# Kernel optimization log

Measured on AMD Instinct MI355X. Metric: run time of the kernel, lower is better.

Reference implementation:

```python
import jax, jax.numpy as jnp
import numpy as np

N_NODES = 100000
N_EDGES = 1280000
D_IN = 64
D_HID = 128
D_OUT = 64


def sage_conv(x, src, dst, W_l, b_l, W_r, n_nodes):
    # PyG SAGEConv (aggr='mean', root_weight=True):
    #   out_i = W_l @ mean_{j in N(i)} x_j + b_l + W_r @ x_i
    msg = x[src]  # [E, d] gather of source-node features
    agg = jax.ops.segment_sum(msg, dst, num_segments=n_nodes)  # [N, d]
    cnt = jax.ops.segment_sum(jnp.ones((src.shape[0], 1), x.dtype), dst,
                              num_segments=n_nodes)  # [N, 1]
    mean = agg / jnp.maximum(cnt, 1.0)  # zero-neighbor nodes -> 0 (matches scatter-mean)
    return mean @ W_l.T + b_l + x @ W_r.T


def setup_inputs() -> dict:
    key = jax.random.key(0)
    ks = jax.random.split(key, 8)
    x = jax.random.normal(ks[0], (N_NODES, D_IN), dtype=jnp.float32)
    edge_index = jax.random.randint(ks[1], (2, N_EDGES), 0, N_NODES, dtype=jnp.int64)
    s = 0.05
    W_l1 = jax.random.normal(ks[2], (D_HID, D_IN), dtype=jnp.float32) * s
    b_l1 = jnp.zeros((D_HID,), dtype=jnp.float32)
    W_r1 = jax.random.normal(ks[3], (D_HID, D_IN), dtype=jnp.float32) * s
    W_l2 = jax.random.normal(ks[4], (D_OUT, D_HID), dtype=jnp.float32) * s
    b_l2 = jnp.zeros((D_OUT,), dtype=jnp.float32)
    W_r2 = jax.random.normal(ks[5], (D_OUT, D_HID), dtype=jnp.float32) * s
    return {"x": x, "edge_index": edge_index,
            "W_l1": W_l1, "b_l1": b_l1, "W_r1": W_r1,
            "W_l2": W_l2, "b_l2": b_l2, "W_r2": W_r2}


def reference(x, edge_index, W_l1, b_l1, W_r1, W_l2, b_l2, W_r2):
    src, dst = edge_index[0], edge_index[1]
    n = x.shape[0]
    h = sage_conv(x, src, dst, W_l1, b_l1, W_r1, n)
    h = jax.nn.relu(h)
    out = sage_conv(h, src, dst, W_l2, b_l2, W_r2, n)
    return out
```

## Files before the change

kernel.cpp:

```cpp
#include <hip/hip_runtime.h>
#include <cstdint>
#include <cstddef>

typedef __attribute__((ext_vector_type(8))) short short8;
typedef __attribute__((ext_vector_type(4))) float floatx4;

static constexpr int DIN  = 64;
static constexpr int DHID = 128;
static constexpr int BSH  = 7;
static constexpr int BNODES = 1 << BSH;
static constexpr int TILE = 8192;
static constexpr int CAP  = 4096;
static constexpr unsigned SENT = 0xFFFFFFFFu;

__device__ inline short f2bf(float f) {
  unsigned u = __float_as_uint(f);
  u += 0x7FFF + ((u >> 16) & 1);
  return (short)(u >> 16);
}
__device__ inline float bf2f(short s) {
  return __uint_as_float(((unsigned)(unsigned short)s) << 16);
}

__global__ __launch_bounds__(256) void prep_kernel(const float* __restrict__ x,
    const float* __restrict__ Wl1, const float* __restrict__ Wr1,
    const float* __restrict__ Wl2, const float* __restrict__ Wr2,
    short* __restrict__ xb, short* __restrict__ wc1, short* __restrict__ wc2,
    int* __restrict__ bcur, int nz,
    int nx, int gx)
{
  int b = blockIdx.x, t = threadIdx.x;
  if (b < gx) {
    int i0 = (b * 256 + t) * 8;
    if (i0 < nx) {
      floatx4 f0 = *(const floatx4*)&x[i0];
      floatx4 f1 = *(const floatx4*)&x[i0 + 4];
      short8 o;
      o[0]=f2bf(f0[0]); o[1]=f2bf(f0[1]); o[2]=f2bf(f0[2]); o[3]=f2bf(f0[3]);
      o[4]=f2bf(f1[0]); o[5]=f2bf(f1[1]); o[6]=f2bf(f1[2]); o[7]=f2bf(f1[3]);
      *(short8*)&xb[i0] = o;
    }
  } else if (b < gx + 32) {
    int wb = b - gx;
    int idx = ((wb & 15) * 256 + t) * 4;
    int n = idx >> 7, k = idx & 127;
    const float* src;
    if (wb < 16) src = (k < 64) ? &Wl1[n * 64 + k] : &Wr1[n * 64 + (k - 64)];
    else         src = (n < 64) ? &Wl2[n * 128 + k] : &Wr2[(n - 64) * 128 + k];
    floatx4 f = *(const floatx4*)src;
    short* dst = (wb < 16 ? wc1 : wc2) + idx;
    dst[0]=f2bf(f[0]); dst[1]=f2bf(f[1]); dst[2]=f2bf(f[2]); dst[3]=f2bf(f[3]);
  } else {
    for (int i = t; i < nz; i += 256) bcur[i] = 0;
  }
}

__global__ __launch_bounds__(256) void partition_kernel(const void* edges, long long nmax,
                                                        int* __restrict__ bucket_cursor,
                                                        int* __restrict__ real_cnt,
                                                        unsigned* __restrict__ packed, int E, int NB) {
  __shared__ unsigned sval[TILE];
  __shared__ unsigned saux[TILE];
  __shared__ int hist[1024];
  __shared__ int gb[1024];
  __shared__ int smode;
  int t = threadIdx.x;
  int base = blockIdx.x * TILE;
  int cnt_here = E - base; if (cnt_here > TILE) cnt_here = TILE;
  for (int i = t; i < NB; i += 256) hist[i] = 0;
  if (t == 0) smode = 1;
  __syncthreads();
  {
    const long long* e64 = (const long long*)edges;
    int nchk = E < 256 ? E : 256;
    bool ok = true;
    for (int i = t; i < nchk; i += 256) {
      long long v = e64[i];
      if (v < 0 || v >= nmax) ok = false;
    }
    if (!ok) smode = 0;
  }
  __syncthreads();
  bool m64 = (smode != 0);
  #pragma unroll 4
  for (int c = 0; c < TILE / 256; ++c) {
    int idx = c * 256 + t;
    if (idx < cnt_here) {
      int i = base + idx;
      int s, d;
      if (m64) { const long long* e = (const long long*)edges; s = (int)e[i]; d = (int)e[(size_t)E + i]; }
      else     { const int*       e = (const int*)edges;       s = e[i];      d = e[(size_t)E + i]; }
      int b = d >> BSH;
      int rank = atomicAdd(&hist[b], 1);
      sval[idx] = ((unsigned)(d & (BNODES - 1)) << 17) | (unsigned)s;
      saux[idx] = ((unsigned)b << 13) | (unsigned)rank;
    }
  }
  __syncthreads();
  for (int b = t; b < NB; b += 256) {
    int cnt = hist[b];
    int gbase = 0;
    if (cnt > 0) {
      int pad = (cnt + 15) & ~15;
      gbase = b * CAP + atomicAdd(&bucket_cursor[b], pad);
      atomicAdd(&real_cnt[b], cnt);
      for (int j = cnt; j < pad; ++j) packed[gbase + j] = SENT;
    }
    gb[b] = gbase;
  }
  __syncthreads();
  #pragma unroll 4
  for (int c = 0; c < TILE / 256; ++c) {
    int idx = c * 256 + t;
    if (idx < cnt_here) {
      unsigned a = saux[idx];
      packed[gb[a >> 13] + (a & 0x1FFFu)] = sval[idx];
    }
  }
}

__global__ __launch_bounds__(256) void bucket_scan_kernel(const int* __restrict__ real_cnt,
                                                          int* __restrict__ ebase,
                                                          int* __restrict__ row_ptr,
                                                          int NB, int N, int E) {
  int t = threadIdx.x;
  int i0 = t * 4;
  int v[4]; int s = 0;
  #pragma unroll
  for (int c = 0; c < 4; ++c) { int idx = i0 + c; v[c] = (idx < NB) ? real_cnt[idx] : 0; s += v[c]; }
  int lane = t & 63, w = t >> 6;
  int val = s;
  #pragma unroll
  for (int off = 1; off < 64; off <<= 1) {
    int u = __shfl_up(val, off, 64);
    if (lane >= off) val += u;
  }
  __shared__ int wsum[4];
  if (lane == 63) wsum[w] = val;
  __syncthreads();
  int wpre = 0;
  for (int ww = 0; ww < w; ++ww) wpre += wsum[ww];
  int run = wpre + val - s;
  #pragma unroll
  for (int c = 0; c < 4; ++c) { int idx = i0 + c; if (idx < NB) ebase[idx] = run; run += v[c]; }
  if (t == 0) row_ptr[N] = E;
}

__global__ __launch_bounds__(256) void bucket_sort_kernel(const unsigned* __restrict__ packed,
                                                          const int* __restrict__ bucket_cursor,
                                                          const int* __restrict__ ebase,
                                                          int* __restrict__ row_ptr,
                                                          int* __restrict__ sorted_src, int N) {
  __shared__ int nhist[BNODES];
  __shared__ int cur[BNODES];
  __shared__ int wsum[4];
  int b = blockIdx.x, t = threadIdx.x;
  int n0 = b << BSH;
  int nn = N - n0; if (nn > BNODES) nn = BNODES;
  if (t < BNODES) nhist[t] = 0;
  __syncthreads();
  int rbeg = b * CAP, rcnt = bucket_cursor[b];
  for (int i = t; i < rcnt; i += 256) {
    unsigned p = packed[rbeg + i];
    if (p != SENT) atomicAdd(&nhist[p >> 17], 1);
  }
  __syncthreads();
  int lane = t & 63, w = t >> 6;
  int v = (t < BNODES) ? nhist[t] : 0;
  int val = v;
  #pragma unroll
  for (int off = 1; off < 64; off <<= 1) {
    int u = __shfl_up(val, off, 64);
    if (lane >= off) val += u;
  }
  if (lane == 63) wsum[w] = val;
  __syncthreads();
  int pre = (w == 1) ? wsum[0] : 0;
  int excl = pre + val - v;
  int eb = ebase[b];
  if (t < nn) { row_ptr[n0 + t] = eb + excl; cur[t] = eb + excl; }
  __syncthreads();
  for (int i = t; i < rcnt; i += 256) {
    unsigned p = packed[rbeg + i];
    if (p != SENT) {
      int pos = atomicAdd(&cur[p >> 17], 1);
      sorted_src[pos] = (int)(p & 0x1FFFFu);
    }
  }
}

template <bool EPI>
__global__ __launch_bounds__(256) void agg_bf16_kernel(const short* __restrict__ feat,
                                                       const int* __restrict__ row_ptr,
                                                       const int* __restrict__ srcs,
                                                       const float* __restrict__ rbuf,
                                                       const float* __restrict__ bias,
                                                       short* __restrict__ outb,
                                                       float* __restrict__ outf, int N) {
  int node = blockIdx.x * 32 + (threadIdx.x >> 3);
  if (node >= N) return;
  int c = threadIdx.x & 7;
  const short* fbase = feat + c * 8;
  int beg = row_ptr[node], end = row_ptr[node + 1];
  float acc[8];
  #pragma unroll
  for (int j = 0; j < 8; ++j) acc[j] = 0.f;
  int e = beg;
  for (; e + 4 <= end; e += 4) {
    int s0 = srcs[e], s1 = srcs[e + 1], s2 = srcs[e + 2], s3 = srcs[e + 3];
    short8 v0 = *(const short8*)&fbase[(size_t)s0 * 64];
    short8 v1 = *(const short8*)&fbase[(size_t)s1 * 64];
    short8 v2 = *(const short8*)&fbase[(size_t)s2 * 64];
    short8 v3 = *(const short8*)&fbase[(size_t)s3 * 64];
    #pragma unroll
    for (int j = 0; j < 8; ++j)
      acc[j] += (bf2f(v0[j]) + bf2f(v1[j])) + (bf2f(v2[j]) + bf2f(v3[j]));
  }
  for (; e < end; ++e) {
    short8 v = *(const short8*)&fbase[(size_t)srcs[e] * 64];
    #pragma unroll
    for (int j = 0; j < 8; ++j) acc[j] += bf2f(v[j]);
  }
  float inv = 1.f / fmaxf((float)(end - beg), 1.f);
  if (!EPI) {
    short8 o;
    #pragma unroll
    for (int j = 0; j < 8; ++j) o[j] = f2bf(acc[j] * inv);
    *(short8*)&outb[(size_t)node * 64 + c * 8] = o;
  } else {
    floatx4 b0 = *(const floatx4*)&bias[c * 8];
    floatx4 b1 = *(const floatx4*)&bias[c * 8 + 4];
    floatx4 r0 = *(const floatx4*)&rbuf[(size_t)node * 64 + c * 8];
    floatx4 r1 = *(const floatx4*)&rbuf[(size_t)node * 64 + c * 8 + 4];
    floatx4 o0, o1;
    #pragma unroll
    for (int j = 0; j < 4; ++j) {
      o0[j] = acc[j] * inv + b0[j] + r0[j];
      o1[j] = acc[4 + j] * inv + b1[j] + r1[j];
    }
    *(floatx4*)&outf[(size_t)node * 64 + c * 8]     = o0;
    *(floatx4*)&outf[(size_t)node * 64 + c * 8 + 4] = o1;
  }
}

__global__ __launch_bounds__(256) void fused_gemm_kernel(
    const short* __restrict__ Aa, const short* __restrict__ Ab,
    const short* __restrict__ wc1, const short* __restrict__ wc2,
    const float* __restrict__ bias1,
    short* __restrict__ Cg, float* __restrict__ Cr, int M)
{
  __shared__ short Ws[128][136];
  __shared__ short Hs[64][136];
  int t = threadIdx.x;
  #pragma unroll
  for (int i = 0; i < 8; ++i) {
    int idx = i * 256 + t;
    int r = idx >> 4, c8 = (idx & 15) * 8;
    *(short8*)&Ws[r][c8] = *(const short8*)&wc1[r * 128 + c8];
  }
  __syncthreads();
  int wv = t >> 6, lane = t & 63, q = lane >> 4, l15 = lane & 15;
  int m0 = blockIdx.x * 64 + wv * 16;
  int row = m0 + l15;
  bool rowok = row < M;
  floatx4 acc[8];
  #pragma unroll
  for (int nt = 0; nt < 8; ++nt) acc[nt] = (floatx4){0.f, 0.f, 0.f, 0.f};
  #pragma unroll
  for (int ko = 0; ko < 4; ++ko) {
    const short* Asrc = (ko < 2) ? Aa : Ab;
    short8 a = {0, 0, 0, 0, 0, 0, 0, 0};
    if (rowok) a = *(const short8*)&Asrc[(size_t)row * 64 + (ko & 1) * 32 + q * 8];
    #pragma unroll
    for (int nt = 0; nt < 8; ++nt) {
      short8 b = *(const short8*)&Ws[nt * 16 + l15][ko * 32 + q * 8];
      acc[nt] = __builtin_amdgcn_mfma_f32_16x16x32_bf16(a, b, acc[nt], 0, 0, 0);
    }
  }
  #pragma unroll
  for (int nt = 0; nt < 8; ++nt) {
    int n = nt * 16 + l15;
    float bv = bias1[n];
    #pragma unroll
    for (int r2 = 0; r2 < 4; ++r2) {
      int lr = wv * 16 + q * 4 + r2;
      float v = fmaxf(acc[nt][r2] + bv, 0.f);
      Hs[lr][n] = f2bf(v);
    }
  }
  __syncthreads();
  #pragma unroll
  for (int i = 0; i < 8; ++i) {
    int idx = i * 256 + t;
    int r = idx >> 4, c8 = (idx & 15) * 8;
    *(short8*)&Ws[r][c8] = *(const short8*)&wc2[r * 128 + c8];
  }
  __syncthreads();
  #pragma unroll
  for (int nt = 0; nt < 8; ++nt) acc[nt] = (floatx4){0.f, 0.f, 0.f, 0.f};
  #pragma unroll
  for (int ko = 0; ko < 4; ++ko) {
    short8 a = *(const short8*)&Hs[wv * 16 + l15][ko * 32 + q * 8];
    #pragma unroll
    for (int nt = 0; nt < 8; ++nt) {
      short8 b = *(const short8*)&Ws[nt * 16 + l15][ko * 32 + q * 8];
      acc[nt] = __builtin_amdgcn_mfma_f32_16x16x32_bf16(a, b, acc[nt], 0, 0, 0);
    }
  }
  #pragma unroll
  for (int nt = 0; nt < 8; ++nt) {
    int n = nt * 16 + l15;
    #pragma unroll
    for (int r2 = 0; r2 < 4; ++r2) {
      int mr = m0 + q * 4 + r2;
      if (mr >= M) continue;
      float v = acc[nt][r2];
      if (nt < 4) Cg[(size_t)mr * 64 + n] = f2bf(v);
      else        Cr[(size_t)mr * 64 + (n - 64)] = v;
    }
  }
}

extern "C" void kernel_launch(void* const* d_in, const int* in_sizes, int n_in,
                              void* d_out, int out_size, void* d_ws, size_t ws_size,
                              hipStream_t stream) {
  const float* x   = (const float*)d_in[0];
  const void*  ei  = d_in[1];
  const float* Wl1 = (const float*)d_in[2];
  const float* bl1 = (const float*)d_in[3];
  const float* Wr1 = (const float*)d_in[4];
  const float* Wl2 = (const float*)d_in[5];
  const float* bl2 = (const float*)d_in[6];
  const float* Wr2 = (const float*)d_in[7];
  int N = in_sizes[0] / DIN;
  int E = in_sizes[1] / 2;
  int NB = (N + BNODES - 1) / BNODES;

  char* w = (char*)d_ws;
  size_t off = 0;
  auto alloc = [&](size_t bytes) -> void* {
    void* p = w + off;
    off += (bytes + 255) & ~(size_t)255;
    return p;
  };
  int*      bcur       = (int*)alloc((size_t)NB * 8);
  int*      rcnt       = bcur + NB;
  int*      ebase      = (int*)alloc((size_t)NB * 4);
  int*      row_ptr    = (int*)alloc(((size_t)N + 1) * 4);
  unsigned* packed     = (unsigned*)alloc((size_t)NB * CAP * 4);
  int*      sorted_src = (int*)alloc((size_t)E * 4);
  short*    xb         = (short*)alloc((size_t)N * 64 * 2);
  short*    meanb      = (short*)alloc((size_t)N * 64 * 2);
  float*    rbuf       = (float*)alloc((size_t)N * 64 * 4);
  short*    wc1        = (short*)alloc(128 * 128 * 2);
  short*    wc2        = (short*)alloc(128 * 128 * 2);
  (void)ws_size; (void)n_in; (void)out_size;

  int nx = N * DIN;
  int gx = (nx / 8 + 255) / 256;
  prep_kernel<<<gx + 33, 256, 0, stream>>>(x, Wl1, Wr1, Wl2, Wr2, xb, wc1, wc2,
                                           bcur, NB * 2, nx, gx);

  int gP = (E + TILE - 1) / TILE;
  partition_kernel<<<gP, 256, 0, stream>>>(ei, (long long)N, bcur, rcnt, packed, E, NB);
  bucket_scan_kernel<<<1, 256, 0, stream>>>(rcnt, ebase, row_ptr, NB, N, E);
  bucket_sort_kernel<<<NB, 256, 0, stream>>>(packed, bcur, ebase, row_ptr, sorted_src, N);

  int gN32 = (N + 31) / 32;
  agg_bf16_kernel<false><<<gN32, 256, 0, stream>>>(xb, row_ptr, sorted_src, nullptr, nullptr, meanb, nullptr, N);

  int gm = (N + 63) / 64;
  fused_gemm_kernel<<<gm, 256, 0, stream>>>(meanb, xb, wc1, wc2, bl1, meanb, rbuf, N);

  agg_bf16_kernel<true><<<gN32, 256, 0, stream>>>(meanb, row_ptr, sorted_src, rbuf, bl2, nullptr, (float*)d_out, N);
}
```

Baseline: 207.4 us.

## Fuse prep into partition, fold bucket scan into sort, widen aggregation gather

Merges the bf16 conversion of x and the weights into the partition kernel launch and replaces the kernel-based zeroing of the bucket counters with a memset. The single-block bucket scan is removed, and each sort block instead recomputes its base offset by reducing the counts of all earlier buckets. The aggregation loop now gathers 8 neighbours per iteration with vectorised index loads and paired bf16-to-float conversion. Fewer launches and more memory-level parallelism are the aim, at the cost of redundant prefix reductions in every sort block and higher register pressure.

```diff
diff --git a/kernel.cpp b/kernel.cpp
--- a/kernel.cpp
+++ b/kernel.cpp
@@ -4,6 +4,8 @@
 
 typedef __attribute__((ext_vector_type(8))) short short8;
 typedef __attribute__((ext_vector_type(4))) float floatx4;
+typedef __attribute__((ext_vector_type(2))) float floatx2;
+typedef __attribute__((ext_vector_type(4))) int intx4;
 
 static constexpr int DIN  = 64;
 static constexpr int DHID = 128;
@@ -21,51 +23,55 @@
 __device__ inline float bf2f(short s) {
   return __uint_as_float(((unsigned)(unsigned short)s) << 16);
 }
-
-__global__ __launch_bounds__(256) void prep_kernel(const float* __restrict__ x,
+__device__ inline floatx2 bfpair(unsigned u) {
+  floatx2 r;
+  r[0] = __uint_as_float(u << 16);
+  r[1] = __uint_as_float(u & 0xFFFF0000u);
+  return r;
+}
+
+__global__ __launch_bounds__(256) void part_prep_kernel(const void* edges, long long nmax,
+    int* __restrict__ bucket_cursor, int* __restrict__ real_cnt,
+    unsigned* __restrict__ packed, int E, int NB,
+    const float* __restrict__ x,
     const float* __restrict__ Wl1, const float* __restrict__ Wr1,
     const float* __restrict__ Wl2, const float* __restrict__ Wr2,
     short* __restrict__ xb, short* __restrict__ wc1, short* __restrict__ wc2,
-    int* __restrict__ bcur, int nz,
-    int nx, int gx)
+    int nx, int gP, int gx)
 {
-  int b = blockIdx.x, t = threadIdx.x;
-  if (b < gx) {
-    int i0 = (b * 256 + t) * 8;
-    if (i0 < nx) {
-      floatx4 f0 = *(const floatx4*)&x[i0];
-      floatx4 f1 = *(const floatx4*)&x[i0 + 4];
-      short8 o;
-      o[0]=f2bf(f0[0]); o[1]=f2bf(f0[1]); o[2]=f2bf(f0[2]); o[3]=f2bf(f0[3]);
-      o[4]=f2bf(f1[0]); o[5]=f2bf(f1[1]); o[6]=f2bf(f1[2]); o[7]=f2bf(f1[3]);
-      *(short8*)&xb[i0] = o;
-    }
-  } else if (b < gx + 32) {
-    int wb = b - gx;
-    int idx = ((wb & 15) * 256 + t) * 4;
-    int n = idx >> 7, k = idx & 127;
-    const float* src;
-    if (wb < 16) src = (k < 64) ? &Wl1[n * 64 + k] : &Wr1[n * 64 + (k - 64)];
-    else         src = (n < 64) ? &Wl2[n * 128 + k] : &Wr2[(n - 64) * 128 + k];
-    floatx4 f = *(const floatx4*)src;
-    short* dst = (wb < 16 ? wc1 : wc2) + idx;
-    dst[0]=f2bf(f[0]); dst[1]=f2bf(f[1]); dst[2]=f2bf(f[2]); dst[3]=f2bf(f[3]);
-  } else {
-    for (int i = t; i < nz; i += 256) bcur[i] = 0;
-  }
-}
-
-__global__ __launch_bounds__(256) void partition_kernel(const void* edges, long long nmax,
-                                                        int* __restrict__ bucket_cursor,
-                                                        int* __restrict__ real_cnt,
-                                                        unsigned* __restrict__ packed, int E, int NB) {
   __shared__ unsigned sval[TILE];
   __shared__ unsigned saux[TILE];
   __shared__ int hist[1024];
   __shared__ int gb[1024];
   __shared__ int smode;
   int t = threadIdx.x;
-  int base = blockIdx.x * TILE;
+  int blk = blockIdx.x;
+  if (blk >= gP) {
+    int b = blk - gP;
+    if (b < gx) {
+      int i0 = (b * 256 + t) * 8;
+      if (i0 < nx) {
+        floatx4 f0 = *(const floatx4*)&x[i0];
+        floatx4 f1 = *(const floatx4*)&x[i0 + 4];
+        short8 o;
+        o[0]=f2bf(f0[0]); o[1]=f2bf(f0[1]); o[2]=f2bf(f0[2]); o[3]=f2bf(f0[3]);
+        o[4]=f2bf(f1[0]); o[5]=f2bf(f1[1]); o[6]=f2bf(f1[2]); o[7]=f2bf(f1[3]);
+        *(short8*)&xb[i0] = o;
+      }
+    } else {
+      int wb = b - gx;
+      int idx = ((wb & 15) * 256 + t) * 4;
+      int n = idx >> 7, k = idx & 127;
+      const float* src;
+      if (wb < 16) src = (k < 64) ? &Wl1[n * 64 + k] : &Wr1[n * 64 + (k - 64)];
+      else         src = (n < 64) ? &Wl2[n * 128 + k] : &Wr2[(n - 64) * 128 + k];
+      floatx4 f = *(const floatx4*)src;
+      short* dst = (wb < 16 ? wc1 : wc2) + idx;
+      dst[0]=f2bf(f[0]); dst[1]=f2bf(f[1]); dst[2]=f2bf(f[2]); dst[3]=f2bf(f[3]);
+    }
+    return;
+  }
+  int base = blk * TILE;
   int cnt_here = E - base; if (cnt_here > TILE) cnt_here = TILE;
   for (int i = t; i < NB; i += 256) hist[i] = 0;
   if (t == 0) smode = 1;
@@ -119,46 +125,27 @@
   }
 }
 
-__global__ __launch_bounds__(256) void bucket_scan_kernel(const int* __restrict__ real_cnt,
-                                                          int* __restrict__ ebase,
-                                                          int* __restrict__ row_ptr,
-                                                          int NB, int N, int E) {
-  int t = threadIdx.x;
-  int i0 = t * 4;
-  int v[4]; int s = 0;
-  #pragma unroll
-  for (int c = 0; c < 4; ++c) { int idx = i0 + c; v[c] = (idx < NB) ? real_cnt[idx] : 0; s += v[c]; }
-  int lane = t & 63, w = t >> 6;
-  int val = s;
-  #pragma unroll
-  for (int off = 1; off < 64; off <<= 1) {
-    int u = __shfl_up(val, off, 64);
-    if (lane >= off) val += u;
-  }
-  __shared__ int wsum[4];
-  if (lane == 63) wsum[w] = val;
-  __syncthreads();
-  int wpre = 0;
-  for (int ww = 0; ww < w; ++ww) wpre += wsum[ww];
-  int run = wpre + val - s;
-  #pragma unroll
-  for (int c = 0; c < 4; ++c) { int idx = i0 + c; if (idx < NB) ebase[idx] = run; run += v[c]; }
-  if (t == 0) row_ptr[N] = E;
-}
-
 __global__ __launch_bounds__(256) void bucket_sort_kernel(const unsigned* __restrict__ packed,
                                                           const int* __restrict__ bucket_cursor,
-                                                          const int* __restrict__ ebase,
+                                                          const int* __restrict__ real_cnt,
                                                           int* __restrict__ row_ptr,
-                                                          int* __restrict__ sorted_src, int N) {
+                                                          int* __restrict__ sorted_src, int N, int E) {
   __shared__ int nhist[BNODES];
   __shared__ int cur[BNODES];
   __shared__ int wsum[4];
+  __shared__ int redsum[4];
   int b = blockIdx.x, t = threadIdx.x;
+  int partial = 0;
+  for (int i = t; i < b; i += 256) partial += real_cnt[i];
+  #pragma unroll
+  for (int off = 1; off < 64; off <<= 1) partial += __shfl_xor(partial, off, 64);
+  if ((t & 63) == 0) redsum[t >> 6] = partial;
+  if (t < BNODES) nhist[t] = 0;
+  if (b == 0 && t == 0) row_ptr[N] = E;
+  __syncthreads();
+  int eb = redsum[0] + redsum[1] + redsum[2] + redsum[3];
   int n0 = b << BSH;
   int nn = N - n0; if (nn > BNODES) nn = BNODES;
-  if (t < BNODES) nhist[t] = 0;
-  __syncthreads();
   int rbeg = b * CAP, rcnt = bucket_cursor[b];
   for (int i = t; i < rcnt; i += 256) {
     unsigned p = packed[rbeg + i];
@@ -177,7 +164,6 @@
   __syncthreads();
   int pre = (w == 1) ? wsum[0] : 0;
   int excl = pre + val - v;
-  int eb = ebase[b];
   if (t < nn) { row_ptr[n0 + t] = eb + excl; cur[t] = eb + excl; }
   __syncthreads();
   for (int i = t; i < rcnt; i += 256) {
@@ -202,25 +188,64 @@
   int c = threadIdx.x & 7;
   const short* fbase = feat + c * 8;
   int beg = row_ptr[node], end = row_ptr[node + 1];
-  float acc[8];
-  #pragma unroll
-  for (int j = 0; j < 8; ++j) acc[j] = 0.f;
+  floatx2 acc2[4];
+  #pragma unroll
+  for (int k = 0; k < 4; ++k) acc2[k] = (floatx2){0.f, 0.f};
   int e = beg;
+  for (; e + 8 <= end; e += 8) {
+    intx4 sa = *(const intx4*)&srcs[e];
+    intx4 sb = *(const intx4*)&srcs[e + 4];
+    short8 v0 = *(const short8*)&fbase[(size_t)sa[0] * 64];
+    short8 v1 = *(const short8*)&fbase[(size_t)sa[1] * 64];
+    short8 v2 = *(const short8*)&fbase[(size_t)sa[2] * 64];
+    short8 v3 = *(const short8*)&fbase[(size_t)sa[3] * 64];
+    short8 v4 = *(const short8*)&fbase[(size_t)sb[0] * 64];
+    short8 v5 = *(const short8*)&fbase[(size_t)sb[1] * 64];
+    short8 v6 = *(const short8*)&fbase[(size_t)sb[2] * 64];
+    short8 v7 = *(const short8*)&fbase[(size_t)sb[3] * 64];
+    const unsigned* u0 = (const unsigned*)&v0;
+    const unsigned* u1 = (const unsigned*)&v1;
+    const unsigned* u2 = (const unsigned*)&v2;
+    const unsigned* u3 = (const unsigned*)&v3;
+    const unsigned* u4 = (const unsigned*)&v4;
+    const unsigned* u5 = (const unsigned*)&v5;
+    const unsigned* u6 = (const unsigned*)&v6;
+    const unsigned* u7 = (const unsigned*)&v7;
+    #pragma unroll
+    for (int k = 0; k < 4; ++k) {
+      floatx2 s01 = bfpair(u0[k]) + bfpair(u1[k]);
+      floatx2 s23 = bfpair(u2[k]) + bfpair(u3[k]);
+      floatx2 s45 = bfpair(u4[k]) + bfpair(u5[k]);
+      floatx2 s67 = bfpair(u6[k]) + bfpair(u7[k]);
+      acc2[k] += (s01 + s23) + (s45 + s67);
+    }
+  }
   for (; e + 4 <= end; e += 4) {
-    int s0 = srcs[e], s1 = srcs[e + 1], s2 = srcs[e + 2], s3 = srcs[e + 3];
-    short8 v0 = *(const short8*)&fbase[(size_t)s0 * 64];
-    short8 v1 = *(const short8*)&fbase[(size_t)s1 * 64];
-    short8 v2 = *(const short8*)&fbase[(size_t)s2 * 64];
-    short8 v3 = *(const short8*)&fbase[(size_t)s3 * 64];
-    #pragma unroll
-    for (int j = 0; j < 8; ++j)
-      acc[j] += (bf2f(v0[j]) + bf2f(v1[j])) + (bf2f(v2[j]) + bf2f(v3[j]));
+    intx4 sa = *(const intx4*)&srcs[e];
+    short8 v0 = *(const short8*)&fbase[(size_t)sa[0] * 64];
+    short8 v1 = *(const short8*)&fbase[(size_t)sa[1] * 64];
+    short8 v2 = *(const short8*)&fbase[(size_t)sa[2] * 64];
+    short8 v3 = *(const short8*)&fbase[(size_t)sa[3] * 64];
+    const unsigned* u0 = (const unsigned*)&v0;
+    const unsigned* u1 = (const unsigned*)&v1;
+    const unsigned* u2 = (const unsigned*)&v2;
+    const unsigned* u3 = (const unsigned*)&v3;
+    #pragma unroll
+    for (int k = 0; k < 4; ++k) {
+      floatx2 s01 = bfpair(u0[k]) + bfpair(u1[k]);
+      floatx2 s23 = bfpair(u2[k]) + bfpair(u3[k]);
+      acc2[k] += s01 + s23;
+    }
   }
   for (; e < end; ++e) {
     short8 v = *(const short8*)&fbase[(size_t)srcs[e] * 64];
-    #pragma unroll
-    for (int j = 0; j < 8; ++j) acc[j] += bf2f(v[j]);
-  }
+    const unsigned* u = (const unsigned*)&v;
+    #pragma unroll
+    for (int k = 0; k < 4; ++k) acc2[k] += bfpair(u[k]);
+  }
+  float acc[8];
+  #pragma unroll
+  for (int k = 0; k < 4; ++k) { acc[2 * k] = acc2[k][0]; acc[2 * k + 1] = acc2[k][1]; }
   float inv = 1.f / fmaxf((float)(end - beg), 1.f);
   if (!EPI) {
     short8 o;
@@ -345,7 +370,6 @@
   };
   int*      bcur       = (int*)alloc((size_t)NB * 8);
   int*      rcnt       = bcur + NB;
-  int*      ebase      = (int*)alloc((size_t)NB * 4);
   int*      row_ptr    = (int*)alloc(((size_t)N + 1) * 4);
   unsigned* packed     = (unsigned*)alloc((size_t)NB * CAP * 4);
   int*      sorted_src = (int*)alloc((size_t)E * 4);
@@ -356,15 +380,16 @@
   short*    wc2        = (short*)alloc(128 * 128 * 2);
   (void)ws_size; (void)n_in; (void)out_size;
 
+  hipMemsetAsync(bcur, 0, (size_t)NB * 8, stream);
+
   int nx = N * DIN;
   int gx = (nx / 8 + 255) / 256;
-  prep_kernel<<<gx + 33, 256, 0, stream>>>(x, Wl1, Wr1, Wl2, Wr2, xb, wc1, wc2,
-                                           bcur, NB * 2, nx, gx);
-
   int gP = (E + TILE - 1) / TILE;
-  partition_kernel<<<gP, 256, 0, stream>>>(ei, (long long)N, bcur, rcnt, packed, E, NB);
-  bucket_scan_kernel<<<1, 256, 0, stream>>>(rcnt, ebase, row_ptr, NB, N, E);
-  bucket_sort_kernel<<<NB, 256, 0, stream>>>(packed, bcur, ebase, row_ptr, sorted_src, N);
+  part_prep_kernel<<<gP + gx + 32, 256, 0, stream>>>(ei, (long long)N, bcur, rcnt, packed,
+                                                     E, NB, x, Wl1, Wr1, Wl2, Wr2,
+                                                     xb, wc1, wc2, nx, gP, gx);
+
+  bucket_sort_kernel<<<NB, 256, 0, stream>>>(packed, bcur, rcnt, row_ptr, sorted_src, N, E);
 
   int gN32 = (N + 31) / 32;
   agg_bf16_kernel<false><<<gN32, 256, 0, stream>>>(xb, row_ptr, sorted_src, nullptr, nullptr, meanb, nullptr, N);
```

Result: no change. 203.5 us (-1.9%).
